# Performance work log

Measured on AMD Instinct MI355X. Metric: run time of the kernel, lower is better.

Reference implementation:

```python
import jax, jax.numpy as jnp
import numpy as np

B, P, E, D, A = 128, 196, 2048, 512, 512


def setup_inputs() -> dict:
    key = jax.random.key(0)
    ks = jax.random.split(key, 8)
    s = lambda fan_in: 1.0 / np.sqrt(fan_in)
    return {
        "encoder_out": jax.random.normal(ks[0], (B, P, E), jnp.float32),
        "decoder_hidden": jax.random.normal(ks[1], (B, D), jnp.float32),
        "We": jax.random.uniform(ks[2], (E, A), jnp.float32, -s(E), s(E)),
        "be": jax.random.uniform(ks[3], (A,), jnp.float32, -s(E), s(E)),
        "Wd": jax.random.uniform(ks[4], (D, A), jnp.float32, -s(D), s(D)),
        "bd": jax.random.uniform(ks[5], (A,), jnp.float32, -s(D), s(D)),
        "Wf": jax.random.uniform(ks[6], (A, 1), jnp.float32, -s(A), s(A)),
        "bf": jax.random.uniform(ks[7], (1,), jnp.float32, -s(A), s(A)),
    }


def reference(encoder_out, decoder_hidden, We, be, Wd, bd, Wf, bf):
    # att1: [B, P, A]
    att1 = jnp.einsum("bpe,ea->bpa", encoder_out, We) + be
    # att2: [B, A]
    att2 = decoder_hidden @ Wd + bd
    # additive attention scores: [B, P]
    att = (jax.nn.relu(att1 + att2[:, None, :]) @ Wf + bf)[..., 0]
    alpha = jax.nn.softmax(att, axis=1)  # softmax over pixels
    # weighted sum over pixels: [B, E]
    awe = jnp.einsum("bpe,bp->be", encoder_out, alpha)
    return awe, alpha
```

## Files before the change

kernel.cpp:

```cpp
#include <hip/hip_runtime.h>
#include <hip/hip_bf16.h>

typedef __attribute__((ext_vector_type(2))) unsigned int u32x2;
typedef __attribute__((ext_vector_type(4))) float f32x4;
typedef __attribute__((ext_vector_type(8))) short s16x8;

#define B_  128
#define P_  196
#define E_  2048
#define D_  512
#define A_  512
#define M_  (B_*P_)
#define MT  112

#define WAIT_LGKM0() asm volatile("s_waitcnt lgkmcnt(0)" ::: "memory")

__global__ void we_conv_kernel(const float* __restrict__ We,
                               unsigned short* __restrict__ WeTf) {
  __shared__ float tile[32][33];
  const int tx = threadIdx.x, ty = threadIdx.y;
  const int a0 = blockIdx.x * 32, e0 = blockIdx.y * 32;
  tile[ty][tx] = We[(e0 + ty) * A_ + a0 + tx];
  __syncthreads();
  const float v = tile[tx][ty];
  const unsigned int u = __float_as_uint(v);
  const unsigned short r = (unsigned short)((u + 0x7fffu + ((u >> 16) & 1u)) >> 16);
  const int a = a0 + ty;
  const int kt = blockIdx.y;
  const int q = tx >> 3, j = tx & 7;
  const int nf = a >> 4, fr = a & 15;
  WeTf[kt * 16384 + nf * 512 + (q * 16 + fr) * 8 + j] = r;
}

__global__ void att2_kernel(const float* __restrict__ h, const float* __restrict__ Wd,
                            const float* __restrict__ bd, const float* __restrict__ be,
                            float* __restrict__ att2pb) {
  const int b = blockIdx.x;
  const int t = threadIdx.x;
  __shared__ float hs[D_];
  hs[t] = h[b * D_ + t];
  hs[t + 256] = h[b * D_ + t + 256];
  __syncthreads();
  float a0 = 0.f, a1 = 0.f;
  for (int d = 0; d < D_; ++d) {
    const float hv = hs[d];
    a0 = fmaf(hv, Wd[d * A_ + t], a0);
    a1 = fmaf(hv, Wd[d * A_ + t + 256], a1);
  }
  att2pb[b * A_ + t] = a0 + bd[t] + be[t];
  att2pb[b * A_ + t + 256] = a1 + bd[t + 256] + be[t + 256];
}

__device__ inline unsigned pk2(float a, float b) {
  union { __hip_bfloat162 h; unsigned u; } cv;
  cv.h = __float22bfloat162_rn(make_float2(a, b));
  return cv.u;
}
__device__ __forceinline__ s16x8 ldsr(const unsigned short* p) {
  return *(const s16x8*)p;
}
#define MF(a, b, c) c = __builtin_amdgcn_mfma_f32_16x16x32_bf16(a, b, c, 0, 0, 0)

__launch_bounds__(1024, 4)
__global__ void score_kernel(const float* __restrict__ enc,
                             const unsigned short* __restrict__ WeTf,
                             const float* __restrict__ att2pb,
                             const float* __restrict__ Wf,
                             float* __restrict__ att_part) {
  __shared__ unsigned short Ahs[3][128 * 32];

  const int bid = blockIdx.x;
  const int m0 = bid * MT;

  const int t = threadIdx.x;
  const int lane = t & 63, w = t >> 6;
  const int wn = w * 32;

  const int ar = t >> 3, ac4 = t & 7;
  const int arc = ar < MT ? ar : MT - 1;
  const float* aptr = enc + (size_t)(m0 + arc) * E_ + ac4 * 4;
  const int awz = (ar * 32 + ac4 * 4) ^ ((ar & 7) << 3);

  const unsigned short* bfp = WeTf + (w * 2) * 512 + lane * 8;

  const int q = lane >> 4, fr = lane & 15;
  const int fx = (fr & 7) << 3;
  int fa[7];
#pragma unroll
  for (int i = 0; i < 7; ++i) fa[i] = ((i * 16 + fr) * 32 + q * 8) ^ fx;

  const f32x4 zero = {0.f, 0.f, 0.f, 0.f};
  f32x4 acc[7][2];
#pragma unroll
  for (int mi = 0; mi < 7; ++mi) {
    acc[mi][0] = zero;
    acc[mi][1] = zero;
  }

  unsigned short *bAc = &Ahs[0][0], *bA1 = &Ahs[1][0], *bA2 = &Ahs[2][0];
  f32x4 aC, aN;
  s16x8 bE0, bE1, bO0, bO1;

  {
    aC = *(const f32x4*)(aptr);
    bE0 = ldsr(bfp);
    bE1 = ldsr(bfp + 512);
    aN = *(const f32x4*)(aptr + 32);
    bO0 = ldsr(bfp + 16384);
    bO1 = ldsr(bfp + 16384 + 512);
    u32x2 av; av[0] = pk2(aC[0], aC[1]); av[1] = pk2(aC[2], aC[3]);
    *(u32x2*)(bAc + awz) = av;
    aC = aN;
    WAIT_LGKM0();
    __builtin_amdgcn_s_barrier();
  }

#define SUBITER(TT, BB0, BB1) {                                               \
    aN = *(const f32x4*)(aptr + ((TT) + 2) * 32);                             \
    __builtin_amdgcn_s_setprio(1);                                            \
    _Pragma("unroll")                                                         \
    for (int mi = 0; mi < 7; ++mi) {                                          \
      const s16x8 fah = ldsr(bAc + fa[mi]);                                   \
      MF(fah, BB0, acc[mi][0]);                                               \
      MF(fah, BB1, acc[mi][1]);                                               \
    }                                                                         \
    __builtin_amdgcn_s_setprio(0);                                            \
    BB0 = ldsr(bfp + ((TT) + 2) * 16384);                                     \
    BB1 = ldsr(bfp + ((TT) + 2) * 16384 + 512);                               \
    u32x2 av; av[0] = pk2(aC[0], aC[1]); av[1] = pk2(aC[2], aC[3]);           \
    *(u32x2*)(bA1 + awz) = av;                                                \
    aC = aN;                                                                  \
    WAIT_LGKM0();                                                             \
    __builtin_amdgcn_s_barrier();                                             \
    unsigned short* tmp_ = bAc; bAc = bA1; bA1 = bA2; bA2 = tmp_;             \
  }

  for (int it = 0; it < 62; it += 2) {
    SUBITER(it, bE0, bE1)
    SUBITER(it + 1, bO0, bO1)
  }
#undef SUBITER

  {
    __builtin_amdgcn_s_setprio(1);
#pragma unroll
    for (int mi = 0; mi < 7; ++mi) {
      const s16x8 fah = ldsr(bAc + fa[mi]);
      MF(fah, bE0, acc[mi][0]);
      MF(fah, bE1, acc[mi][1]);
    }
    __builtin_amdgcn_s_setprio(0);
    u32x2 av; av[0] = pk2(aC[0], aC[1]); av[1] = pk2(aC[2], aC[3]);
    *(u32x2*)(bA1 + awz) = av;
    WAIT_LGKM0();
    __builtin_amdgcn_s_barrier();
    unsigned short* tmp_ = bAc; bAc = bA1; bA1 = bA2; bA2 = tmp_;
  }

  {
#pragma unroll
    for (int mi = 0; mi < 7; ++mi) {
      const s16x8 fah = ldsr(bAc + fa[mi]);
      MF(fah, bO0, acc[mi][0]);
      MF(fah, bO1, acc[mi][1]);
    }
  }

  const int colL = wn + fr;
  const float wf0 = Wf[colL], wf1 = Wf[colL + 16];
#pragma unroll
  for (int mi = 0; mi < 7; ++mi) {
    const int rowb = m0 + mi * 16 + (q << 2);
#pragma unroll
    for (int r = 0; r < 4; ++r) {
      const int row = rowb + r;
      const int bb = row / P_;
      const float* a2 = att2pb + bb * A_ + colL;
      float s = fmaxf(acc[mi][0][r] + a2[0], 0.f) * wf0
              + fmaxf(acc[mi][1][r] + a2[16], 0.f) * wf1;
#pragma unroll
      for (int off = 1; off < 16; off <<= 1) s += __shfl_xor(s, off);
      if (fr == 0) att_part[row * 16 + w] = s;
    }
  }
}

__global__ void softmax_awe_kernel(const float* __restrict__ enc,
                                   const float* __restrict__ att_part,
                                   float* __restrict__ out) {
  const int bid = blockIdx.x;
  const int b = bid >> 1, ch = bid & 1;
  const int t = threadIdx.x;
  __shared__ float sm[256];
  __shared__ float alpha_s[P_];

  float av = -1e30f;
  if (t < P_) {
    const float* apt = att_part + (b * P_ + t) * 16;
    float s = 0.f;
#pragma unroll
    for (int i = 0; i < 16; ++i) s += apt[i];
    av = s;
  }
  sm[t] = av;
  __syncthreads();
  for (int st = 128; st > 0; st >>= 1) {
    if (t < st) sm[t] = fmaxf(sm[t], sm[t + st]);
    __syncthreads();
  }
  const float mx = sm[0];
  __syncthreads();
  float ev = 0.f;
  if (t < P_) ev = __expf(av - mx);
  sm[t] = ev;
  __syncthreads();
  for (int st = 128; st > 0; st >>= 1) {
    if (t < st) sm[t] += sm[t + st];
    __syncthreads();
  }
  const float denom = sm[0];
  const float al = ev / denom;
  if (t < P_) {
    alpha_s[t] = al;
    if (ch == 0) out[B_ * E_ + b * P_ + t] = al;
  }
  __syncthreads();

  const int e0 = ch * 1024 + t * 4;
  const float* ebase = enc + (size_t)b * P_ * E_ + e0;
  f32x4 acc = {0.f, 0.f, 0.f, 0.f};
  for (int p = 0; p < P_; ++p) {
    const f32x4 v = *(const f32x4*)(ebase + (size_t)p * E_);
    const float a = alpha_s[p];
    acc.x += a * v.x; acc.y += a * v.y; acc.z += a * v.z; acc.w += a * v.w;
  }
  *(f32x4*)(out + b * E_ + e0) = acc;
}

extern "C" void kernel_launch(void* const* d_in, const int* in_sizes, int n_in,
                              void* d_out, int out_size, void* d_ws, size_t ws_size,
                              hipStream_t stream) {
  const float* enc = (const float*)d_in[0];
  const float* h   = (const float*)d_in[1];
  const float* We  = (const float*)d_in[2];
  const float* be  = (const float*)d_in[3];
  const float* Wd  = (const float*)d_in[4];
  const float* bd  = (const float*)d_in[5];
  const float* Wf  = (const float*)d_in[6];
  float* out = (float*)d_out;

  float* att2pb = (float*)d_ws;
  float* att_part = att2pb + B_ * A_;
  unsigned short* WeTf = (unsigned short*)(att_part + M_ * 16);

  we_conv_kernel<<<dim3(A_ / 32, E_ / 32), dim3(32, 32), 0, stream>>>(We, WeTf);
  att2_kernel<<<B_, 256, 0, stream>>>(h, Wd, bd, be, att2pb);
  score_kernel<<<M_ / MT, 1024, 0, stream>>>(enc, WeTf, att2pb, Wf, att_part);
  softmax_awe_kernel<<<B_ * 2, 256, 0, stream>>>(enc, att_part, out);
}
```

Before: 119.0 us.

## Double K-step per barrier in score GEMM and split awe kernel finer

The score kernel now stages a 64-wide K slice of the encoder tile per iteration instead of 32. Each thread loads and converts 8 floats and writes 16 bytes to LDS, which halves the number of barriers and loop iterations. The LDS buffers double in size. The softmax/weighted-sum kernel splits E into four chunks per batch instead of two, giving more blocks for the memory-bound reduction at the cost of recomputing the softmax twice as often.

```diff
diff --git a/kernel.cpp b/kernel.cpp
--- a/kernel.cpp
+++ b/kernel.cpp
@@ -1,8 +1,9 @@
 #include <hip/hip_runtime.h>
 #include <hip/hip_bf16.h>
 
-typedef __attribute__((ext_vector_type(2))) unsigned int u32x2;
+typedef __attribute__((ext_vector_type(2))) float f32x2;
 typedef __attribute__((ext_vector_type(4))) float f32x4;
+typedef __attribute__((ext_vector_type(4))) unsigned int u32x4;
 typedef __attribute__((ext_vector_type(8))) short s16x8;
 
 #define B_  128
@@ -56,6 +57,14 @@
   cv.h = __float22bfloat162_rn(make_float2(a, b));
   return cv.u;
 }
+__device__ inline u32x4 cvt8(const f32x4 lo, const f32x4 hi) {
+  u32x4 r;
+  r[0] = pk2(lo[0], lo[1]);
+  r[1] = pk2(lo[2], lo[3]);
+  r[2] = pk2(hi[0], hi[1]);
+  r[3] = pk2(hi[2], hi[3]);
+  return r;
+}
 __device__ __forceinline__ s16x8 ldsr(const unsigned short* p) {
   return *(const s16x8*)p;
 }
@@ -67,7 +76,7 @@
                              const float* __restrict__ att2pb,
                              const float* __restrict__ Wf,
                              float* __restrict__ att_part) {
-  __shared__ unsigned short Ahs[3][128 * 32];
+  __shared__ unsigned short Ahs[3][128 * 64];
 
   const int bid = blockIdx.x;
   const int m0 = bid * MT;
@@ -76,18 +85,21 @@
   const int lane = t & 63, w = t >> 6;
   const int wn = w * 32;
 
-  const int ar = t >> 3, ac4 = t & 7;
+  const int ar = t >> 3, ac8 = t & 7;
   const int arc = ar < MT ? ar : MT - 1;
-  const float* aptr = enc + (size_t)(m0 + arc) * E_ + ac4 * 4;
-  const int awz = (ar * 32 + ac4 * 4) ^ ((ar & 7) << 3);
+  const float* aptr = enc + (size_t)(m0 + arc) * E_ + ac8 * 8;
+  const int awz = (ar * 64 + ac8 * 8) ^ ((ar & 7) << 3);
 
   const unsigned short* bfp = WeTf + (w * 2) * 512 + lane * 8;
 
   const int q = lane >> 4, fr = lane & 15;
   const int fx = (fr & 7) << 3;
-  int fa[7];
-#pragma unroll
-  for (int i = 0; i < 7; ++i) fa[i] = ((i * 16 + fr) * 32 + q * 8) ^ fx;
+  int fa[2][7];
+#pragma unroll
+  for (int ks = 0; ks < 2; ++ks)
+#pragma unroll
+    for (int i = 0; i < 7; ++i)
+      fa[ks][i] = ((i * 16 + fr) * 64 + ks * 32 + q * 8) ^ fx;
 
   const f32x4 zero = {0.f, 0.f, 0.f, 0.f};
   f32x4 acc[7][2];
@@ -98,72 +110,74 @@
   }
 
   unsigned short *bAc = &Ahs[0][0], *bA1 = &Ahs[1][0], *bA2 = &Ahs[2][0];
-  f32x4 aC, aN;
+  f32x4 aC0, aC1, aN0, aN1;
   s16x8 bE0, bE1, bO0, bO1;
 
   {
-    aC = *(const f32x4*)(aptr);
+    aC0 = *(const f32x4*)(aptr);
+    aC1 = *(const f32x4*)(aptr + 4);
     bE0 = ldsr(bfp);
     bE1 = ldsr(bfp + 512);
-    aN = *(const f32x4*)(aptr + 32);
+    aN0 = *(const f32x4*)(aptr + 64);
+    aN1 = *(const f32x4*)(aptr + 68);
     bO0 = ldsr(bfp + 16384);
     bO1 = ldsr(bfp + 16384 + 512);
-    u32x2 av; av[0] = pk2(aC[0], aC[1]); av[1] = pk2(aC[2], aC[3]);
-    *(u32x2*)(bAc + awz) = av;
-    aC = aN;
+    *(u32x4*)(bAc + awz) = cvt8(aC0, aC1);
+    aC0 = aN0; aC1 = aN1;
     WAIT_LGKM0();
     __builtin_amdgcn_s_barrier();
   }
 
-#define SUBITER(TT, BB0, BB1) {                                               \
-    aN = *(const f32x4*)(aptr + ((TT) + 2) * 32);                             \
-    __builtin_amdgcn_s_setprio(1);                                            \
-    _Pragma("unroll")                                                         \
-    for (int mi = 0; mi < 7; ++mi) {                                          \
-      const s16x8 fah = ldsr(bAc + fa[mi]);                                   \
-      MF(fah, BB0, acc[mi][0]);                                               \
-      MF(fah, BB1, acc[mi][1]);                                               \
-    }                                                                         \
-    __builtin_amdgcn_s_setprio(0);                                            \
-    BB0 = ldsr(bfp + ((TT) + 2) * 16384);                                     \
-    BB1 = ldsr(bfp + ((TT) + 2) * 16384 + 512);                               \
-    u32x2 av; av[0] = pk2(aC[0], aC[1]); av[1] = pk2(aC[2], aC[3]);           \
-    *(u32x2*)(bA1 + awz) = av;                                                \
-    aC = aN;                                                                  \
-    WAIT_LGKM0();                                                             \
-    __builtin_amdgcn_s_barrier();                                             \
-    unsigned short* tmp_ = bAc; bAc = bA1; bA1 = bA2; bA2 = tmp_;             \
-  }
-
-  for (int it = 0; it < 62; it += 2) {
-    SUBITER(it, bE0, bE1)
-    SUBITER(it + 1, bO0, bO1)
-  }
-#undef SUBITER
+  for (int it = 0; it < 31; ++it) {
+    const int kpre = (it < 30 ? it + 2 : 31) * 64;
+    aN0 = *(const f32x4*)(aptr + kpre);
+    aN1 = *(const f32x4*)(aptr + kpre + 4);
+    const unsigned short* bnext = bfp + (size_t)(it + 1) * 32768;
+
+    __builtin_amdgcn_s_setprio(1);
+#pragma unroll
+    for (int mi = 0; mi < 7; ++mi) {
+      const s16x8 fah = ldsr(bAc + fa[0][mi]);
+      MF(fah, bE0, acc[mi][0]);
+      MF(fah, bE1, acc[mi][1]);
+    }
+    __builtin_amdgcn_s_setprio(0);
+    bE0 = ldsr(bnext);
+    bE1 = ldsr(bnext + 512);
+
+    __builtin_amdgcn_s_setprio(1);
+#pragma unroll
+    for (int mi = 0; mi < 7; ++mi) {
+      const s16x8 fah = ldsr(bAc + fa[1][mi]);
+      MF(fah, bO0, acc[mi][0]);
+      MF(fah, bO1, acc[mi][1]);
+    }
+    __builtin_amdgcn_s_setprio(0);
+    bO0 = ldsr(bnext + 16384);
+    bO1 = ldsr(bnext + 16384 + 512);
+
+    *(u32x4*)(bA1 + awz) = cvt8(aC0, aC1);
+    aC0 = aN0; aC1 = aN1;
+    WAIT_LGKM0();
+    __builtin_amdgcn_s_barrier();
+    unsigned short* tmp = bAc; bAc = bA1; bA1 = bA2; bA2 = tmp;
+  }
 
   {
     __builtin_amdgcn_s_setprio(1);
 #pragma unroll
     for (int mi = 0; mi < 7; ++mi) {
-      const s16x8 fah = ldsr(bAc + fa[mi]);
+      const s16x8 fah = ldsr(bAc + fa[0][mi]);
       MF(fah, bE0, acc[mi][0]);
       MF(fah, bE1, acc[mi][1]);
     }
-    __builtin_amdgcn_s_setprio(0);
-    u32x2 av; av[0] = pk2(aC[0], aC[1]); av[1] = pk2(aC[2], aC[3]);
-    *(u32x2*)(bA1 + awz) = av;
-    WAIT_LGKM0();
-    __builtin_amdgcn_s_barrier();
-    unsigned short* tmp_ = bAc; bAc = bA1; bA1 = bA2; bA2 = tmp_;
-  }
-
-  {
-#pragma unroll
-    for (int mi = 0; mi < 7; ++mi) {
-      const s16x8 fah = ldsr(bAc + fa[mi]);
+#pragma unroll
+    for (int mi = 0; mi < 7; ++mi) {
+      const s16x8 fah = ldsr(bAc + fa[1][mi]);
       MF(fah, bO0, acc[mi][0]);
       MF(fah, bO1, acc[mi][1]);
     }
+    __builtin_amdgcn_s_setprio(0);
   }
 
   const int colL = wn + fr;
@@ -189,7 +203,7 @@
                                    const float* __restrict__ att_part,
                                    float* __restrict__ out) {
   const int bid = blockIdx.x;
-  const int b = bid >> 1, ch = bid & 1;
+  const int b = bid >> 2, ch = bid & 3;
   const int t = threadIdx.x;
   __shared__ float sm[256];
   __shared__ float alpha_s[P_];
@@ -226,15 +240,16 @@
   }
   __syncthreads();
 
-  const int e0 = ch * 1024 + t * 4;
+  const int e0 = ch * 512 + t * 2;
   const float* ebase = enc + (size_t)b * P_ * E_ + e0;
-  f32x4 acc = {0.f, 0.f, 0.f, 0.f};
+  f32x2 acc = {0.f, 0.f};
   for (int p = 0; p < P_; ++p) {
-    const f32x4 v = *(const f32x4*)(ebase + (size_t)p * E_);
+    const f32x2 v = *(const f32x2*)(ebase + (size_t)p * E_);
     const float a = alpha_s[p];
-    acc.x += a * v.x; acc.y += a * v.y; acc.z += a * v.z; acc.w += a * v.w;
-  }
-  *(f32x4*)(out + b * E_ + e0) = acc;
+    acc.x += a * v.x;
+    acc.y += a * v.y;
+  }
+  *(f32x2*)(out + b * E_ + e0) = acc;
 }
 
 extern "C" void kernel_launch(void* const* d_in, const int* in_sizes, int n_in,
@@ -256,5 +271,5 @@
   we_conv_kernel<<<dim3(A_ / 32, E_ / 32), dim3(32, 32), 0, stream>>>(We, WeTf);
   att2_kernel<<<B_, 256, 0, stream>>>(h, Wd, bd, be, att2pb);
   score_kernel<<<M_ / MT, 1024, 0, stream>>>(enc, WeTf, att2pb, Wf, att_part);
-  softmax_awe_kernel<<<B_ * 2, 256, 0, stream>>>(enc, att_part, out);
-}
+  softmax_awe_kernel<<<B_ * 4, 256, 0, stream>>>(enc, att_part, out);
+}
```

Result: no change. 119.8 us (+0.7%).
